# Kernel optimization log

Hardware: AMD Instinct MI355X
Metric: run time of the kernel (lower is better)

Reference implementation:

```python
import jax, jax.numpy as jnp
import numpy as np

UP = 512      # up_size
RADIUS = 60   # revise crop radius -> 120x120 squares
COEF = 1.5    # COM threshold coefficient
DOT = 4       # intensity-adjust circle radius
B = 16
M = 4
BASE = 128


def _affine_grid(theta, H, W):
    # torch F.affine_grid, align_corners=False. theta: (2,3) -> grid (H,W,2) with (x,y)
    xs = (2.0 * jnp.arange(W, dtype=jnp.float32) + 1.0) / W - 1.0
    ys = (2.0 * jnp.arange(H, dtype=jnp.float32) + 1.0) / H - 1.0
    X, Y = jnp.meshgrid(xs, ys)  # (H,W), X varies along width
    base = jnp.stack([X, Y, jnp.ones_like(X)], axis=-1)  # (H,W,3)
    return base @ theta.T  # (H,W,2)


def _gs_one(im, gr):
    # torch F.grid_sample, bilinear, zero padding, align_corners=False
    # im: (C,H,W), gr: (Hg,Wg,2) -> (C,Hg,Wg)
    C, H, W = im.shape
    x = ((gr[..., 0] + 1.0) * W - 1.0) * 0.5
    y = ((gr[..., 1] + 1.0) * H - 1.0) * 0.5
    x0 = jnp.floor(x)
    y0 = jnp.floor(y)
    wx = x - x0
    wy = y - y0

    def tap(ix, iy, w):
        valid = (ix >= 0) & (ix < W) & (iy >= 0) & (iy < H)
        ii = jnp.clip(iy, 0, H - 1).astype(jnp.int32)
        jj = jnp.clip(ix, 0, W - 1).astype(jnp.int32)
        return im[:, ii, jj] * (jnp.where(valid, w, 0.0))[None]

    return (tap(x0, y0, (1 - wx) * (1 - wy))
            + tap(x0 + 1, y0, wx * (1 - wy))
            + tap(x0, y0 + 1, (1 - wx) * wy)
            + tap(x0 + 1, y0 + 1, wx * wy))


_grid_sample = jax.vmap(_gs_one)  # (B,C,H,W),(B,Hg,Wg,2)->(B,C,Hg,Wg)


def _inv2x3(theta):
    # append [0,0,1], invert 3x3, keep top 2 rows (as in Joint.forward)
    n = theta.shape[0]
    bottom = jnp.broadcast_to(jnp.array([[0.0, 0.0, 1.0]], jnp.float32), (n, 1, 3))
    full = jnp.concatenate([theta, bottom], axis=1)
    return jnp.linalg.inv(full)[:, :2]


def _com(img, mask, coef):
    # center_of_mass: threshold = coef * mean over mask, intensity-weighted centroid
    H, W = img.shape
    msum = jnp.maximum(mask.sum(), 1.0)
    thr = (img.sum() / msum) * coef
    w = jnp.where(img > thr, img, 0.0)
    tot = w.sum() + 1e-8
    cx = (w.sum(axis=1) * jnp.arange(H, dtype=img.dtype)).sum() / tot  # row
    cy = (w.sum(axis=0) * jnp.arange(W, dtype=img.dtype)).sum() / tot  # col
    return cx, cy


def _revise(image, masks_rot, inv_theta, adj, radius, coef, dot):
    # revise_size_on_affine_gpu with adj_para given and pare_reverse=True
    d = 2 * radius
    yy, xx = jnp.meshgrid(jnp.arange(d), jnp.arange(d), indexing='ij')
    small_sq = ((yy - radius) ** 2 + (xx - radius) ** 2) <= dot ** 2  # dot mask

    def per_item(img_i, new_i, mask_i, th_i, a_i):
        cx, cy = _com(new_i, mask_i, coef)
        x0 = jnp.round(cx).astype(jnp.int32) - radius
        y0 = jnp.round(cy).astype(jnp.int32) - radius
        small = jax.lax.dynamic_slice(img_i[0], (x0, y0), (d, d))
        small = jnp.where(small_sq, small / a_i, small)  # pare_reverse=True -> divide
        out = _gs_one(small[None], _affine_grid(th_i, d, d))  # (1,d,d)
        return jax.lax.dynamic_update_slice(img_i, out, (0, x0, y0))

    img = image
    for j in range(masks_rot.shape[0]):
        mj = masks_rot[j]                 # (B,H,W) float 0/1
        new = image[:, 0] * mj            # COM always from original image*mask
        img = jax.vmap(per_item)(img, new, mj, inv_theta, adj)
    return img


def setup_inputs() -> dict:
    key = jax.random.key(0)
    ks = jax.random.split(key, 6)
    predicted_base = jax.random.uniform(ks[0], (B, 1, BASE, BASE), jnp.float32)
    e = 0.05 * jax.random.normal(ks[1], (B, 4), jnp.float32)
    sc = (jnp.zeros((B, 2, 3), jnp.float32)
          .at[:, 0, 0].set(1.0 + e[:, 0]).at[:, 0, 1].set(e[:, 1])
          .at[:, 1, 0].set(e[:, 2]).at[:, 1, 1].set(1.0 + e[:, 3]))
    ang = jax.random.uniform(ks[2], (B,), jnp.float32, -0.2, 0.2)
    rot = (jnp.zeros((B, 2, 3), jnp.float32)
           .at[:, 0, 0].set(jnp.cos(ang)).at[:, 0, 1].set(-jnp.sin(ang))
           .at[:, 1, 0].set(jnp.sin(ang)).at[:, 1, 1].set(jnp.cos(ang)))
    t = jax.random.uniform(ks[3], (B, 2), jnp.float32, -0.05, 0.05)
    tr = (jnp.zeros((B, 2, 3), jnp.float32)
          .at[:, 0, 0].set(1.0).at[:, 1, 1].set(1.0)
          .at[:, 0, 2].set(t[:, 0]).at[:, 1, 2].set(t[:, 1]))
    adj = jax.random.uniform(ks[4], (B,), jnp.float32, 0.9, 1.1)
    centers = [(128, 128), (128, 384), (384, 128), (384, 384)]
    yy, xx = np.meshgrid(np.arange(UP), np.arange(UP), indexing='ij')
    masks = np.stack([((yy - cy) ** 2 + (xx - cx) ** 2 <= 30 ** 2).astype(np.float32)
                      for (cy, cx) in centers])
    return dict(predicted_base=predicted_base, scaler_shear=sc, rotation=rot,
                translation=tr, adj_mask=adj, masks=jnp.asarray(masks))


def reference(predicted_base, scaler_shear, rotation, translation, adj_mask, masks):
    b = predicted_base.shape[0]
    it1 = _inv2x3(scaler_shear)
    it2 = _inv2x3(rotation)
    it3 = _inv2x3(translation)
    base_inp = jax.image.resize(predicted_base, (b, 1, UP, UP), method='linear')
    mk_grid = jax.vmap(lambda th: _affine_grid(th, UP, UP))
    g1, g2, g3 = mk_grid(it1), mk_grid(it2), mk_grid(it3)
    pred_trans = _grid_sample(base_inp, g3)
    pred_rot = _grid_sample(pred_trans, g2)
    pred_input = _grid_sample(pred_rot, g1)
    # rotate masks through grid_2 then grid_1, threshold at 0.5
    new_masks = []
    for j in range(masks.shape[0]):
        bm = jnp.broadcast_to(masks[j][None, None], (b, 1, UP, UP))
        rm = _grid_sample(_grid_sample(bm, g2), g1)
        new_masks.append(rm[:, 0] >= 0.5)
    masks_rot = jnp.stack(new_masks)  # (M,B,UP,UP) bool
    pred_revise = _revise(pred_input, masks_rot.astype(pred_input.dtype), it1,
                          adj_mask, RADIUS, COEF, DOT)
    return (base_inp, pred_input, pred_revise, masks_rot)
```

## Files before the change

### kernel.cpp

```cpp
#include <hip/hip_runtime.h>
#include <math.h>
#include <limits.h>

#define NPIX (512*512)
#define NB 16
#define RAD 60
#define DSZ 120
#define PSTR 121


__device__ __forceinline__ float gs_bilinear(const float* img, int H, int W,
                                             float gx, float gy) {
    float x = ((gx + 1.0f) * (float)W - 1.0f) * 0.5f;
    float y = ((gy + 1.0f) * (float)H - 1.0f) * 0.5f;
    float xf = floorf(x), yf = floorf(y);
    int ix = (int)xf, iy = (int)yf;
    float wx = x - xf, wy = y - yf;
    float v = 0.0f;
    bool vx0 = (ix >= 0) && (ix < W);
    bool vx1 = (ix >= -1) && (ix < W - 1);
    bool vy0 = (iy >= 0) && (iy < H);
    bool vy1 = (iy >= -1) && (iy < H - 1);
    if (vx0 && vy0) v += img[iy*W + ix]         * ((1.0f - wx) * (1.0f - wy));
    if (vx1 && vy0) v += img[iy*W + ix + 1]     * (wx * (1.0f - wy));
    if (vx0 && vy1) v += img[(iy+1)*W + ix]     * ((1.0f - wx) * wy);
    if (vx1 && vy1) v += img[(iy+1)*W + ix + 1] * (wx * wy);
    return v;
}

__device__ __forceinline__ float gs_bilinear_patch(const float* img, float gx, float gy) {
    float x = ((gx + 1.0f) * 120.0f - 1.0f) * 0.5f;
    float y = ((gy + 1.0f) * 120.0f - 1.0f) * 0.5f;
    float xf = floorf(x), yf = floorf(y);
    int ix = (int)xf, iy = (int)yf;
    float wx = x - xf, wy = y - yf;
    float v = 0.0f;
    bool vx0 = (ix >= 0) && (ix < 120);
    bool vx1 = (ix >= -1) && (ix < 119);
    bool vy0 = (iy >= 0) && (iy < 120);
    bool vy1 = (iy >= -1) && (iy < 119);
    if (vx0 && vy0) v += img[iy*PSTR + ix]         * ((1.0f - wx) * (1.0f - wy));
    if (vx1 && vy0) v += img[iy*PSTR + ix + 1]     * (wx * (1.0f - wy));
    if (vx0 && vy1) v += img[(iy+1)*PSTR + ix]     * ((1.0f - wx) * wy);
    if (vx1 && vy1) v += img[(iy+1)*PSTR + ix + 1] * (wx * wy);
    return v;
}


__global__ void k_prep(const float* __restrict__ sc, const float* __restrict__ rot,
                       const float* __restrict__ tr, float* __restrict__ ws_inv,
                       int* __restrict__ bbox, unsigned* __restrict__ occ,
                       int* __restrict__ qcount) {
    int t = threadIdx.x;
    if (t < 48) {
        int m = t >> 4, b = t & 15;
        const float* th = (m == 0 ? sc : (m == 1 ? rot : tr)) + b * 6;
        float a  = th[0], bb = th[1], tx = th[2];
        float c  = th[3], d  = th[4], ty = th[5];
        float L10 = c / a;
        float dp  = d  - L10 * bb;
        float typ = ty - L10 * tx;
        float i10 = (0.0f - L10) / dp;
        float i00 = (1.0f - bb * i10) / a;
        float i11 = 1.0f / dp;
        float i01 = (0.0f - bb * i11) / a;
        float i12 = (0.0f - typ) / dp;
        float i02 = (0.0f - bb * i12 - tx) / a;
        float* o = ws_inv + m * 96 + b * 6;
        o[0] = i00; o[1] = i01; o[2] = i02;
        o[3] = i10; o[4] = i11; o[5] = i12;
    }
    bbox[t] = ((t & 3) < 2) ? INT_MAX : INT_MIN;
    if (t < 128) occ[t] = 0u;
    if (t == 0) *qcount = 0;
}

__global__ void __launch_bounds__(256) k_occ(const float* __restrict__ masks,
                                             unsigned* __restrict__ occ) {
    int tile = blockIdx.x * 4 + (threadIdx.x >> 6);
    int lane = threadIdx.x & 63;
    int j = tile >> 10, t = tile & 1023;
    int ty = t >> 5, tx = t & 31;
    const float* mk = masks + (size_t)j * NPIX;
    int any = 0;
    for (int i = lane; i < 256; i += 64) {
        int py = ty * 16 + (i >> 4), px = tx * 16 + (i & 15);
        if (mk[py * 512 + px] != 0.0f) any = 1;
    }
    unsigned long long m = __ballot(any);
    if (lane == 0 && m) atomicOr(&occ[j * 32 + ty], 1u << tx);
}

__global__ void __launch_bounds__(256) k_otile(const unsigned* __restrict__ occ,
                                               const float* __restrict__ inv1,
                                               const float* __restrict__ inv2,
                                               int* __restrict__ queue,
                                               int* __restrict__ qcount) {
    int idx = blockIdx.x * 256 + threadIdx.x;
    int jb = idx >> 10, tile = idx & 1023;
    int j = jb >> 4, b = jb & 15;
    int ty = tile >> 5, tx = tile & 31;
    const float* t1 = inv1 + b * 6;
    const float* t2 = inv2 + b * 6;
    float xs[2] = { (float)(tx * 16), (float)(tx * 16 + 15) };
    float ys[2] = { (float)(ty * 16), (float)(ty * 16 + 15) };
    float sxmin = 1e30f, sxmax = -1e30f, symin = 1e30f, symax = -1e30f;
    for (int cy = 0; cy < 2; ++cy)
        for (int cx = 0; cx < 2; ++cx) {
            float X = (2.0f * xs[cx] + 1.0f) / 512.0f - 1.0f;
            float Y = (2.0f * ys[cy] + 1.0f) / 512.0f - 1.0f;
            float gx = t1[0] * X + t1[1] * Y + t1[2];
            float gy = t1[3] * X + t1[4] * Y + t1[5];
            float sx = ((gx + 1.0f) * 512.0f - 1.0f) * 0.5f;
            float sy = ((gy + 1.0f) * 512.0f - 1.0f) * 0.5f;
            sxmin = fminf(sxmin, sx); sxmax = fmaxf(sxmax, sx);
            symin = fminf(symin, sy); symax = fmaxf(symax, sy);
        }
    int c0 = max((int)floorf(sxmin) - 1, 0), c1 = min((int)floorf(sxmax) + 2, 511);
    int r0 = max((int)floorf(symin) - 1, 0), r1 = min((int)floorf(symax) + 2, 511);
    bool any = false;
    if (c0 <= c1 && r0 <= r1) {
        float A0 = t2[0], A1 = t2[1], A3 = t2[3], A4 = t2[4];
        float Kx = 0.5f * (-511.0f * (A0 + A1) + 512.0f * t2[2] + 511.0f);
        float Ky = 0.5f * (-511.0f * (A3 + A4) + 512.0f * t2[5] + 511.0f);
        float pxmin = A0 * (A0 >= 0.f ? c0 : c1) + A1 * (A1 >= 0.f ? r0 : r1) + Kx;
        float pxmax = A0 * (A0 >= 0.f ? c1 : c0) + A1 * (A1 >= 0.f ? r1 : r0) + Kx;
        float pymin = A3 * (A3 >= 0.f ? c0 : c1) + A4 * (A4 >= 0.f ? r0 : r1) + Ky;
        float pymax = A3 * (A3 >= 0.f ? c1 : c0) + A4 * (A4 >= 0.f ? r1 : r0) + Ky;
        int xlo = max((int)floorf(pxmin) - 1, 0), xhi = min((int)floorf(pxmax) + 2, 511);
        int ylo = max((int)floorf(pymin) - 1, 0), yhi = min((int)floorf(pymax) + 2, 511);
        if (xlo <= xhi && ylo <= yhi)
            for (int tr = ylo >> 4; tr <= yhi >> 4; ++tr)
                for (int tc = xlo >> 4; tc <= xhi >> 4; ++tc)
                    if ((occ[j * 32 + tr] >> tc) & 1u) any = true;
    }
    if (any) {
        int pos = atomicAdd(qcount, 1);
        queue[pos] = (jb << 10) | tile;
    }
}

__global__ void __launch_bounds__(256) k_zero(float4* __restrict__ p, int n4) {
    int stride = gridDim.x * 256;
    for (int i = blockIdx.x * 256 + threadIdx.x; i < n4; i += stride)
        p[i] = make_float4(0.f, 0.f, 0.f, 0.f);
}

__global__ void __launch_bounds__(256) k_upsample(const float* __restrict__ in,
                                                  float* __restrict__ out) {
    int b = blockIdx.y;
    int p4 = blockIdx.x * 256 + threadIdx.x;
    int p = p4 * 4;
    int y = p >> 9, x0p = p & 511;
    const float* src = in + b * 128 * 128;
    float r[4];
    float sy = (float)y * 0.25f - 0.375f;
    float fy0 = floorf(sy);
    int iy = (int)fy0;
    float fy = sy - fy0;
    int iy0 = min(max(iy, 0), 127), iy1 = min(max(iy + 1, 0), 127);
    #pragma unroll
    for (int k = 0; k < 4; ++k) {
        int x = x0p + k;
        float sx = (float)x * 0.25f - 0.375f;
        float fx0 = floorf(sx);
        int ix = (int)fx0;
        float fx = sx - fx0;
        int ix0 = min(max(ix, 0), 127), ix1 = min(max(ix + 1, 0), 127);
        float v00 = src[iy0 * 128 + ix0], v10 = src[iy0 * 128 + ix1];
        float v01 = src[iy1 * 128 + ix0], v11 = src[iy1 * 128 + ix1];
        r[k] = (v00 * (1.0f - fx) + v10 * fx) * (1.0f - fy)
             + (v01 * (1.0f - fx) + v11 * fx) * fy;
    }
    *(float4*)(out + (size_t)b * NPIX + p) = make_float4(r[0], r[1], r[2], r[3]);
}

__global__ void __launch_bounds__(256) k_gsample(const float* __restrict__ src,
                                                 float* __restrict__ dst,
                                                 float* __restrict__ dst2,
                                                 const float* __restrict__ thetas) {
    int b = blockIdx.y;
    int p4 = blockIdx.x * 256 + threadIdx.x;
    int p = p4 * 4;
    int y = p >> 9, x0p = p & 511;
    const float* th = thetas + b * 6;
    const float* im = src + (size_t)b * NPIX;
    float t0 = th[0], t1 = th[1], t2 = th[2], t3 = th[3], t4 = th[4], t5 = th[5];
    float Y = (2.0f * (float)y + 1.0f) / 512.0f - 1.0f;
    float r[4];
    #pragma unroll
    for (int k = 0; k < 4; ++k) {
        float X = (2.0f * (float)(x0p + k) + 1.0f) / 512.0f - 1.0f;
        float gx = t0 * X + t1 * Y + t2;
        float gy = t3 * X + t4 * Y + t5;
        r[k] = gs_bilinear(im, 512, 512, gx, gy);
    }
    float4 v4 = make_float4(r[0], r[1], r[2], r[3]);
    *(float4*)(dst + (size_t)b * NPIX + p) = v4;
    if (dst2) *(float4*)(dst2 + (size_t)b * NPIX + p) = v4;
}

__device__ __forceinline__ float rm2_val(const float* mk, const float* t2, int cx_, int ry_) {
    float X2 = (2.0f * (float)cx_ + 1.0f) / 512.0f - 1.0f;
    float Y2 = (2.0f * (float)ry_ + 1.0f) / 512.0f - 1.0f;
    float g2x = t2[0] * X2 + t2[1] * Y2 + t2[2];
    float g2y = t2[3] * X2 + t2[4] * Y2 + t2[5];
    return gs_bilinear(mk, 512, 512, g2x, g2y);
}

__global__ void __launch_bounds__(256) k_mask_live(const float* __restrict__ masks,
                                                   float* __restrict__ out3,
                                                   const float* __restrict__ inv1,
                                                   const float* __restrict__ inv2,
                                                   const int* __restrict__ queue,
                                                   const int* __restrict__ qcount,
                                                   int* __restrict__ bbox) {
    __shared__ int sbb[4];
    int n = *qcount;
    for (int q = blockIdx.x; q < n; q += gridDim.x) {
        int e = queue[q];
        int jb = e >> 10, tile = e & 1023;
        if (threadIdx.x == 0) { sbb[0] = INT_MAX; sbb[1] = INT_MAX; sbb[2] = INT_MIN; sbb[3] = INT_MIN; }
        __syncthreads();

        int ty = tile >> 5, tx = tile & 31;
        int y = ty * 16 + (threadIdx.x >> 4);
        int x = tx * 16 + (threadIdx.x & 15);
        int j = jb >> 4, b = jb & 15;
        const float* t1 = inv1 + b * 6;
        const float* t2 = inv2 + b * 6;
        const float* mk = masks + (size_t)j * NPIX;

        float X = (2.0f * (float)x + 1.0f) / 512.0f - 1.0f;
        float Y = (2.0f * (float)y + 1.0f) / 512.0f - 1.0f;
        float gx = t1[0] * X + t1[1] * Y + t1[2];
        float gy = t1[3] * X + t1[4] * Y + t1[5];
        float sx = ((gx + 1.0f) * 512.0f - 1.0f) * 0.5f;
        float sy = ((gy + 1.0f) * 512.0f - 1.0f) * 0.5f;
        float xf = floorf(sx), yf = floorf(sy);
        int ix = (int)xf, iy = (int)yf;
        float wx = sx - xf, wy = sy - yf;

        float v = 0.0f;
        bool vx0 = (ix >= 0) && (ix < 512);
        bool vx1 = (ix >= -1) && (ix < 511);
        bool vy0 = (iy >= 0) && (iy < 512);
        bool vy1 = (iy >= -1) && (iy < 511);
        if (vx0 && vy0) v += rm2_val(mk, t2, ix,     iy    ) * ((1.0f - wx) * (1.0f - wy));
        if (vx1 && vy0) v += rm2_val(mk, t2, ix + 1, iy    ) * (wx * (1.0f - wy));
        if (vx0 && vy1) v += rm2_val(mk, t2, ix,     iy + 1) * ((1.0f - wx) * wy);
        if (vx1 && vy1) v += rm2_val(mk, t2, ix + 1, iy + 1) * (wx * wy);

        float res = 0.0f;
        if (v >= 0.5f) {
            res = 1.0f;
            atomicMin(&sbb[0], y); atomicMin(&sbb[1], x);
            atomicMax(&sbb[2], y); atomicMax(&sbb[3], x);
        }
        out3[(size_t)jb * NPIX + y * 512 + x] = res;

        __syncthreads();
        if (threadIdx.x == 0 && sbb[2] != INT_MIN) {
            atomicMin(&bbox[jb * 4 + 0], sbb[0]);
            atomicMin(&bbox[jb * 4 + 1], sbb[1]);
            atomicMax(&bbox[jb * 4 + 2], sbb[2]);
            atomicMax(&bbox[jb * 4 + 3], sbb[3]);
        }
        __syncthreads();
    }
}

__global__ void __launch_bounds__(256) k_stats(const float* __restrict__ pred,
                                               const float* __restrict__ mrot,
                                               const int* __restrict__ bbox,
                                               int* __restrict__ xy) {
    int jb = blockIdx.x;
    int b = jb & 15;
    int rmin = bbox[jb*4+0], cmin = bbox[jb*4+1], rmax = bbox[jb*4+2], cmax = bbox[jb*4+3];
    const float* img = pred + (size_t)b * NPIX;
    const float* mk  = mrot + (size_t)jb * NPIX;
    int lane = threadIdx.x & 63, w = threadIdx.x >> 6;
    int W = cmax - cmin + 1;
    int total = (rmax >= rmin) ? W * (rmax - rmin + 1) : 0;

    double msum = 0.0, isum = 0.0;
    for (int i = threadIdx.x; i < total; i += 256) {
        int r = rmin + i / W, c = cmin + i % W;
        float m = mk[r * 512 + c];
        if (m != 0.0f) {
            msum += (double)m;
            isum += (double)(img[r * 512 + c] * m);
        }
    }
    for (int o = 32; o > 0; o >>= 1) {
        msum += __shfl_down(msum, o, 64);
        isum += __shfl_down(isum, o, 64);
    }
    __shared__ double s0[4], s1[4], s2[4];
    __shared__ double sthr;
    if (lane == 0) { s0[w] = msum; s1[w] = isum; }
    __syncthreads();
    if (threadIdx.x == 0) {
        double M = s0[0] + s0[1] + s0[2] + s0[3];
        double I = s1[0] + s1[1] + s1[2] + s1[3];
        sthr = (I / fmax(M, 1.0)) * 1.5;
    }
    __syncthreads();
    double t = sthr;

    double wsum = 0.0, sy = 0.0, sx = 0.0;
    for (int i = threadIdx.x; i < total; i += 256) {
        int r = rmin + i / W, c = cmin + i % W;
        float m = mk[r * 512 + c];
        if (m != 0.0f) {
            float v = img[r * 512 + c] * m;
            if ((double)v > t) {
                double vd = (double)v;
                wsum += vd;
                sy += vd * (double)r;
                sx += vd * (double)c;
            }
        }
    }
    for (int o = 32; o > 0; o >>= 1) {
        wsum += __shfl_down(wsum, o, 64);
        sy   += __shfl_down(sy,   o, 64);
        sx   += __shfl_down(sx,   o, 64);
    }
    __syncthreads();
    if (lane == 0) { s0[w] = wsum; s1[w] = sy; s2[w] = sx; }
    __syncthreads();
    if (threadIdx.x == 0) {
        double W_ = s0[0] + s0[1] + s0[2] + s0[3];
        double SY = s1[0] + s1[1] + s1[2] + s1[3];
        double SX = s2[0] + s2[1] + s2[2] + s2[3];
        double tot = W_ + 1e-8;
        int x0 = (int)rint(SY / tot) - RAD;
        int y0 = (int)rint(SX / tot) - RAD;
        x0 = min(max(x0, 0), 512 - DSZ);
        y0 = min(max(y0, 0), 512 - DSZ);
        xy[jb * 2 + 0] = x0;
        xy[jb * 2 + 1] = y0;
    }
}

__device__ __forceinline__ void patch_one(float* __restrict__ im, float* __restrict__ patch,
                                          int x0, int y0, float a,
                                          float t0, float t1, float t2,
                                          float t3, float t4, float t5) {
    for (int t = threadIdx.x; t < DSZ * DSZ; t += 1024) {
        int u = t / DSZ, v = t % DSZ;
        float val = im[(x0 + u) * 512 + (y0 + v)];
        int du = u - RAD, dv = v - RAD;
        if (du * du + dv * dv <= 16) val = val / a;
        patch[u * PSTR + v] = val;
    }
    __syncthreads();
    for (int t = threadIdx.x; t < DSZ * DSZ; t += 1024) {
        int py = t / DSZ, px = t % DSZ;
        float X = (2.0f * (float)px + 1.0f) / 120.0f - 1.0f;
        float Y = (2.0f * (float)py + 1.0f) / 120.0f - 1.0f;
        float gx = t0 * X + t1 * Y + t2;
        float gy = t3 * X + t4 * Y + t5;
        float o = gs_bilinear_patch(patch, gx, gy);
        im[(x0 + py) * 512 + (y0 + px)] = o;
    }
}

__global__ void __launch_bounds__(1024) k_patch(float* __restrict__ img,
                                                const int* __restrict__ xy,
                                                const float* __restrict__ inv1,
                                                const float* __restrict__ adj) {
    __shared__ float patch[DSZ * PSTR];
    int b = blockIdx.x >> 2, j = blockIdx.x & 3;
    int rx[4], ry[4];
    #pragma unroll
    for (int k = 0; k < 4; ++k) {
        rx[k] = xy[(k * 16 + b) * 2 + 0];
        ry[k] = xy[(k * 16 + b) * 2 + 1];
    }
    bool overlap = false;
    #pragma unroll
    for (int i = 0; i < 4; ++i)
        #pragma unroll
        for (int k = 0; k < 4; ++k)
            if (i < k && abs(rx[i] - rx[k]) < DSZ && abs(ry[i] - ry[k]) < DSZ)
                overlap = true;

    float a = adj[b];
    float* im = img + (size_t)b * NPIX;
    const float* th = inv1 + b * 6;
    float t0 = th[0], t1 = th[1], t2 = th[2], t3 = th[3], t4 = th[4], t5 = th[5];

    if (!overlap) {
        patch_one(im, patch, rx[j], ry[j], a, t0, t1, t2, t3, t4, t5);
    } else {
        if (j != 0) return;
        for (int jj = 0; jj < 4; ++jj) {
            patch_one(im, patch, rx[jj], ry[jj], a, t0, t1, t2, t3, t4, t5);
            __threadfence_block();
            __syncthreads();
        }
    }
}


extern "C" void kernel_launch(void* const* d_in, const int* in_sizes, int n_in,
                              void* d_out, int out_size, void* d_ws, size_t ws_size,
                              hipStream_t stream) {
    const float* base  = (const float*)d_in[0];
    const float* sc    = (const float*)d_in[1];
    const float* rot   = (const float*)d_in[2];
    const float* tr    = (const float*)d_in[3];
    const float* adj   = (const float*)d_in[4];
    const float* masks = (const float*)d_in[5];

    float* out  = (float*)d_out;
    float* out0 = out;
    float* out1 = out0 + (size_t)NB * NPIX;
    float* out2 = out1 + (size_t)NB * NPIX;
    float* out3 = out2 + (size_t)NB * NPIX;

    float*    inv1   = (float*)d_ws;
    float*    inv2   = inv1 + 96;
    float*    inv3   = inv1 + 192;
    int*      xy     = (int*)((char*)d_ws + 4096);
    int*      bbox   = (int*)((char*)d_ws + 8192);
    unsigned* occ    = (unsigned*)((char*)d_ws + 12288);
    int*      qcount = (int*)((char*)d_ws + 16128);
    int*      queue  = (int*)((char*)d_ws + 16384);

    dim3 gridImg4(256, NB);

    k_prep<<<1, 256, 0, stream>>>(sc, rot, tr, (float*)d_ws, bbox, occ, qcount);
    k_occ<<<1024, 256, 0, stream>>>(masks, occ);
    k_otile<<<256, 256, 0, stream>>>(occ, inv1, inv2, queue, qcount);
    k_upsample<<<gridImg4, 256, 0, stream>>>(base, out0);

    k_gsample<<<gridImg4, 256, 0, stream>>>(out0, out2, nullptr, inv3);
    k_gsample<<<gridImg4, 256, 0, stream>>>(out2, out3, nullptr, inv2);
    k_gsample<<<gridImg4, 256, 0, stream>>>(out3, out1, out2, inv1);

    k_zero<<<2048, 256, 0, stream>>>((float4*)out3, 64 * NPIX / 4);
    k_mask_live<<<1024, 256, 0, stream>>>(masks, out3, inv1, inv2, queue, qcount, bbox);

    k_stats<<<64, 256, 0, stream>>>(out1, out3, bbox, xy);

    k_patch<<<64, 1024, 0, stream>>>(out2, xy, inv1, adj);
}
```

Before: 278.5 us.

## Tile grid_sample into 32x32 output blocks with LDS-staged source window

The grid-sample kernel now maps each block to a 32x32 output tile, computes the affine bounding box of the source footprint, and stages a 48x48 source window into shared memory when it fits. Bilinear taps then read from LDS instead of scattered global loads, and tiles whose footprint is too large fall back to the direct global path. This trades a cooperative load plus a barrier per block, and some redundant loading of halo pixels, for better locality on gather reads. Output writes are now 2D-tiled rather than row-linear.

After: 247.0 us. 11.3% less time.

```diff
diff --git a/kernel.cpp b/kernel.cpp
--- a/kernel.cpp
+++ b/kernel.cpp
@@ -7,6 +7,8 @@
 #define RAD 60
 #define DSZ 120
 #define PSTR 121
+#define GTS 48
+#define GSTR 49
 
 
 __device__ __forceinline__ float gs_bilinear(const float* img, int H, int W,
@@ -179,25 +181,80 @@
                                                  float* __restrict__ dst,
                                                  float* __restrict__ dst2,
                                                  const float* __restrict__ thetas) {
+    __shared__ float tb[GTS * GSTR];
     int b = blockIdx.y;
-    int p4 = blockIdx.x * 256 + threadIdx.x;
-    int p = p4 * 4;
-    int y = p >> 9, x0p = p & 511;
+    int tile = blockIdx.x;
+    int ox = (tile & 15) * 32, oy = (tile >> 4) * 32;
     const float* th = thetas + b * 6;
+    float t0 = th[0], t1 = th[1], t2 = th[2], t3 = th[3], t4 = th[4], t5 = th[5];
     const float* im = src + (size_t)b * NPIX;
-    float t0 = th[0], t1 = th[1], t2 = th[2], t3 = th[3], t4 = th[4], t5 = th[5];
-    float Y = (2.0f * (float)y + 1.0f) / 512.0f - 1.0f;
+
+    float sxmin = 1e30f, sxmax = -1e30f, symin = 1e30f, symax = -1e30f;
+    #pragma unroll
+    for (int cy = 0; cy < 2; ++cy)
+        #pragma unroll
+        for (int cx = 0; cx < 2; ++cx) {
+            float X = (2.0f * (float)(ox + cx * 31) + 1.0f) / 512.0f - 1.0f;
+            float Y = (2.0f * (float)(oy + cy * 31) + 1.0f) / 512.0f - 1.0f;
+            float gx = t0 * X + t1 * Y + t2;
+            float gy = t3 * X + t4 * Y + t5;
+            float sx = ((gx + 1.0f) * 512.0f - 1.0f) * 0.5f;
+            float sy = ((gy + 1.0f) * 512.0f - 1.0f) * 0.5f;
+            sxmin = fminf(sxmin, sx); sxmax = fmaxf(sxmax, sx);
+            symin = fminf(symin, sy); symax = fmaxf(symax, sy);
+        }
+    int rx0 = (int)floorf(sxmin) - 1;
+    int ry0 = (int)floorf(symin) - 1;
+    bool fits = ((int)floorf(sxmax) + 2 - rx0 < GTS) &&
+                ((int)floorf(symax) + 2 - ry0 < GTS);
+
+    int t = threadIdx.x;
+    int py = oy + (t >> 3);
+    int px0 = ox + (t & 7) * 4;
+    float Y = (2.0f * (float)py + 1.0f) / 512.0f - 1.0f;
     float r[4];
-    #pragma unroll
-    for (int k = 0; k < 4; ++k) {
-        float X = (2.0f * (float)(x0p + k) + 1.0f) / 512.0f - 1.0f;
-        float gx = t0 * X + t1 * Y + t2;
-        float gy = t3 * X + t4 * Y + t5;
-        r[k] = gs_bilinear(im, 512, 512, gx, gy);
+
+    if (fits) {
+        for (int i = t; i < GTS * GTS; i += 256) {
+            int rr = i / GTS, cc = i - rr * GTS;
+            int gy_ = ry0 + rr, gx_ = rx0 + cc;
+            float v = 0.0f;
+            if (gx_ >= 0 && gx_ < 512 && gy_ >= 0 && gy_ < 512)
+                v = im[gy_ * 512 + gx_];
+            tb[rr * GSTR + cc] = v;
+        }
+        __syncthreads();
+        #pragma unroll
+        for (int k = 0; k < 4; ++k) {
+            float X = (2.0f * (float)(px0 + k) + 1.0f) / 512.0f - 1.0f;
+            float gx = t0 * X + t1 * Y + t2;
+            float gy = t3 * X + t4 * Y + t5;
+            float x = ((gx + 1.0f) * 512.0f - 1.0f) * 0.5f;
+            float y = ((gy + 1.0f) * 512.0f - 1.0f) * 0.5f;
+            float xf = floorf(x), yf = floorf(y);
+            int ix = (int)xf, iy = (int)yf;
+            float wx = x - xf, wy = y - yf;
+            int lx = ix - rx0, ly = iy - ry0;
+            float v;
+            v  = tb[ly * GSTR + lx]           * ((1.0f - wx) * (1.0f - wy));
+            v += tb[ly * GSTR + lx + 1]       * (wx * (1.0f - wy));
+            v += tb[(ly + 1) * GSTR + lx]     * ((1.0f - wx) * wy);
+            v += tb[(ly + 1) * GSTR + lx + 1] * (wx * wy);
+            r[k] = v;
+        }
+    } else {
+        #pragma unroll
+        for (int k = 0; k < 4; ++k) {
+            float X = (2.0f * (float)(px0 + k) + 1.0f) / 512.0f - 1.0f;
+            float gx = t0 * X + t1 * Y + t2;
+            float gy = t3 * X + t4 * Y + t5;
+            r[k] = gs_bilinear(im, 512, 512, gx, gy);
+        }
     }
     float4 v4 = make_float4(r[0], r[1], r[2], r[3]);
-    *(float4*)(dst + (size_t)b * NPIX + p) = v4;
-    if (dst2) *(float4*)(dst2 + (size_t)b * NPIX + p) = v4;
+    size_t op = (size_t)b * NPIX + py * 512 + px0;
+    *(float4*)(dst + op) = v4;
+    if (dst2) *(float4*)(dst2 + op) = v4;
 }
 
 __device__ __forceinline__ float rm2_val(const float* mk, const float* t2, int cx_, int ry_) {
@@ -430,16 +487,17 @@
     int*      qcount = (int*)((char*)d_ws + 16128);
     int*      queue  = (int*)((char*)d_ws + 16384);
 
-    dim3 gridImg4(256, NB);
+    dim3 gridUp(256, NB);
+    dim3 gridTile(256, NB);
 
     k_prep<<<1, 256, 0, stream>>>(sc, rot, tr, (float*)d_ws, bbox, occ, qcount);
     k_occ<<<1024, 256, 0, stream>>>(masks, occ);
     k_otile<<<256, 256, 0, stream>>>(occ, inv1, inv2, queue, qcount);
-    k_upsample<<<gridImg4, 256, 0, stream>>>(base, out0);
-
-    k_gsample<<<gridImg4, 256, 0, stream>>>(out0, out2, nullptr, inv3);
-    k_gsample<<<gridImg4, 256, 0, stream>>>(out2, out3, nullptr, inv2);
-    k_gsample<<<gridImg4, 256, 0, stream>>>(out3, out1, out2, inv1);
+    k_upsample<<<gridUp, 256, 0, stream>>>(base, out0);
+
+    k_gsample<<<gridTile, 256, 0, stream>>>(out0, out2, nullptr, inv3);
+    k_gsample<<<gridTile, 256, 0, stream>>>(out2, out3, nullptr, inv2);
+    k_gsample<<<gridTile, 256, 0, stream>>>(out3, out1, out2, inv1);
 
     k_zero<<<2048, 256, 0, stream>>>((float4*)out3, 64 * NPIX / 4);
     k_mask_live<<<1024, 256, 0, stream>>>(masks, out3, inv1, inv2, queue, qcount, bbox);
```
